# Optimization experiments

Measured on AMD Instinct MI355X. Metric: run time of the kernel, lower is better.

## Reference

```python
import jax, jax.numpy as jnp
import numpy as np
from jax import lax

WINDOW_SIZE = 12
POOL = 4  # AvgPool2d(4): 12x12 -> 3x3

# 4 directional 3x3 kernels, stacked as [O=4, I=1, 3, 3]
_KERNELS = np.stack([
    np.array([[0, 0, 0], [-1, 1, 0], [0, 0, 0]], np.float32),  # left
    np.array([[0, 0, 0], [0, 1, -1], [0, 0, 0]], np.float32),  # right
    np.array([[0, -1, 0], [0, 1, 0], [0, 0, 0]], np.float32),  # up
    np.array([[0, 0, 0], [0, 1, 0], [0, -1, 0]], np.float32),  # down
])[:, None, :, :]


def setup_inputs() -> dict:
    key = jax.random.key(0)
    k1, k2 = jax.random.split(key)
    windows_num = 200000
    n = WINDOW_SIZE * WINDOW_SIZE * windows_num
    samples1 = jax.random.uniform(k1, (n, 3), dtype=jnp.float32)
    samples2 = jax.random.uniform(k2, (n, 3), dtype=jnp.float32)
    return {"samples1": samples1, "samples2": samples2, "windows_num": windows_num}


def _to_pooled(samples, windows_num):
    # [W*W*N, C] -> [W, W, N, C] -> [N, C, W, W]
    x = samples.reshape(WINDOW_SIZE, WINDOW_SIZE, windows_num, -1)
    x = jnp.transpose(x, (2, 3, 0, 1))
    # channel mean, keepdim -> [N, 1, W, W]
    m = jnp.mean(x, axis=1, keepdims=True)
    # AvgPool2d(4): [N,1,12,12] -> [N,1,3,3]
    hp = WINDOW_SIZE // POOL
    p = m.reshape(windows_num, 1, hp, POOL, hp, POOL).mean(axis=(3, 5))
    return p


def _dir_grads(x):
    # x: [N,1,3,3]; 4 directional 3x3 convs, padding=1 -> [N,4,3,3]
    k = jnp.asarray(_KERNELS)
    return lax.conv_general_dilated(
        x, k, window_strides=(1, 1), padding=[(1, 1), (1, 1)],
        dimension_numbers=("NCHW", "OIHW", "NCHW"))


def reference(samples1, samples2, windows_num):
    org_pool = _to_pooled(samples1, windows_num)
    enh_pool = _to_pooled(samples2, windows_num)
    d_org = _dir_grads(org_pool)
    d_enh = _dir_grads(enh_pool)
    # squared diff per direction, summed over the 4 directions -> [N,3,3]
    E = jnp.sum((d_org - d_enh) ** 2, axis=1)
    return jnp.mean(E)
```

## Files before the change

### kernel.cpp

```cpp
#include <hip/hip_runtime.h>

typedef float f32x4 __attribute__((ext_vector_type(4)));

__global__ __launch_bounds__(384) void spa_kernel_p6(
    const float* __restrict__ s1, const float* __restrict__ s2,
    float* __restrict__ out, int N, float scale) {
  const int lane = threadIdx.x & 63;
  const int rg   = threadIdx.x >> 6;
  const int g4   = blockIdx.x * 64 + lane;
  const int nG   = N >> 2;

  float P[4][3];
#pragma unroll
  for (int w = 0; w < 4; ++w)
#pragma unroll
    for (int c = 0; c < 3; ++c) P[w][c] = 0.f;

  if (g4 < nG) {
    const size_t stride = (size_t)N * 3u;
    const size_t rowoff = (size_t)12 * stride;
    const float* p1 = s1 + (size_t)g4 * 12u + (size_t)(rg * 2) * rowoff;
    const float* p2 = s2 + (size_t)g4 * 12u + (size_t)(rg * 2) * rowoff;
#pragma unroll 1
    for (int ii = 0; ii < 2; ++ii) {
#pragma unroll
      for (int j = 0; j < 12; ++j) {
        const f32x4* a = (const f32x4*)(p1 + (size_t)j * stride);
        const f32x4* b = (const f32x4*)(p2 + (size_t)j * stride);
        f32x4 a0 = a[0], a1 = a[1], a2 = a[2];
        f32x4 b0 = b[0], b1 = b[1], b2 = b[2];
        float d0 = (a0.x + a0.y + a0.z) - (b0.x + b0.y + b0.z);
        float d1 = (a0.w + a1.x + a1.y) - (b0.w + b1.x + b1.y);
        float d2 = (a1.z + a1.w + a2.x) - (b1.z + b1.w + b2.x);
        float d3 = (a2.y + a2.z + a2.w) - (b2.y + b2.z + b2.w);
        const int pc = j >> 2;
        P[0][pc] += d0;
        P[1][pc] += d1;
        P[2][pc] += d2;
        P[3][pc] += d3;
      }
      p1 += rowoff;
      p2 += rowoff;
    }
  }

  __shared__ float sP[6][64][13];
#pragma unroll
  for (int w = 0; w < 4; ++w)
#pragma unroll
    for (int c = 0; c < 3; ++c) sP[rg][lane][w * 3 + c] = P[w][c];
  __syncthreads();

  if (rg == 0) {
    float e = 0.f;
#pragma unroll
    for (int w = 0; w < 4; ++w) {
      float Q[9];
#pragma unroll
      for (int pr = 0; pr < 3; ++pr)
#pragma unroll
        for (int c = 0; c < 3; ++c)
          Q[pr * 3 + c] = (sP[2 * pr][lane][w * 3 + c] +
                           sP[2 * pr + 1][lane][w * 3 + c]) * (1.0f / 48.0f);
#pragma unroll
      for (int i = 0; i < 3; ++i)
#pragma unroll
        for (int j = 0; j < 3; ++j) {
          float cc = Q[i * 3 + j];
          float l = (j > 0) ? Q[i * 3 + j - 1] : 0.f;
          float r = (j < 2) ? Q[i * 3 + j + 1] : 0.f;
          float u = (i > 0) ? Q[(i - 1) * 3 + j] : 0.f;
          float d = (i < 2) ? Q[(i + 1) * 3 + j] : 0.f;
          float dl = cc - l, dr = cc - r, du = cc - u, dd = cc - d;
          e += dl * dl + dr * dr + du * du + dd * dd;
        }
    }
#pragma unroll
    for (int off = 32; off > 0; off >>= 1) e += __shfl_down(e, off, 64);
    if (lane == 0) atomicAdd(out, e * scale);
  }
}

__global__ __launch_bounds__(512) void spa_kernel_s(
    const float* __restrict__ s1, const float* __restrict__ s2,
    float* __restrict__ out, int N, float scale) {
  const int win = blockIdx.x * 512 + threadIdx.x;
  float P[9];
#pragma unroll
  for (int k = 0; k < 9; ++k) P[k] = 0.f;

  if (win < N) {
    const size_t stride = (size_t)N * 3u;
    const float* p1 = s1 + (size_t)win * 3u;
    const float* p2 = s2 + (size_t)win * 3u;
#pragma unroll 1
    for (int i = 0; i < 12; ++i) {
      const int pr = (i >> 2) * 3;
#pragma unroll
      for (int j = 0; j < 12; ++j) {
        const float* a = p1 + (size_t)j * stride;
        const float* b = p2 + (size_t)j * stride;
        float d = (a[0] + a[1] + a[2]) - (b[0] + b[1] + b[2]);
        P[pr + (j >> 2)] += d;
      }
      p1 += (size_t)12 * stride;
      p2 += (size_t)12 * stride;
    }
  }

#pragma unroll
  for (int k = 0; k < 9; ++k) P[k] *= (1.0f / 48.0f);

  float e = 0.f;
#pragma unroll
  for (int i = 0; i < 3; ++i)
#pragma unroll
    for (int j = 0; j < 3; ++j) {
      float c = P[i * 3 + j];
      float l = (j > 0) ? P[i * 3 + j - 1] : 0.f;
      float r = (j < 2) ? P[i * 3 + j + 1] : 0.f;
      float u = (i > 0) ? P[(i - 1) * 3 + j] : 0.f;
      float d = (i < 2) ? P[(i + 1) * 3 + j] : 0.f;
      float dl = c - l, dr = c - r, du = c - u, dd = c - d;
      e += dl * dl + dr * dr + du * du + dd * dd;
    }

  const int lane = threadIdx.x & 63;
  const int wid = threadIdx.x >> 6;
#pragma unroll
  for (int off = 32; off > 0; off >>= 1) e += __shfl_down(e, off, 64);

  __shared__ float sPart[8];
  if (lane == 0) sPart[wid] = e;
  __syncthreads();
  if (threadIdx.x == 0) {
    float t = 0.f;
#pragma unroll
    for (int w = 0; w < 8; ++w) t += sPart[w];
    atomicAdd(out, t * scale);
  }
}

extern "C" void kernel_launch(void* const* d_in, const int* in_sizes, int n_in,
                              void* d_out, int out_size, void* d_ws, size_t ws_size,
                              hipStream_t stream) {
  const float* s1 = (const float*)d_in[0];
  const float* s2 = (const float*)d_in[1];
  float* out = (float*)d_out;
  int N = in_sizes[0] / (12 * 12 * 3);
  float scale = 1.0f / (9.0f * (float)N);
  hipMemsetAsync(d_out, 0, sizeof(float), stream);
  if ((N & 3) == 0) {
    int nG = N >> 2;
    int blocks = (nG + 63) / 64;
    spa_kernel_p6<<<blocks, 384, 0, stream>>>(s1, s2, out, N, scale);
  } else {
    int blocks = (N + 511) / 512;
    spa_kernel_s<<<blocks, 512, 0, stream>>>(s1, s2, out, N, scale);
  }
}
```

Before: 668.3 us.

## Remap threads to contiguous float4 columns and transpose partial sums through LDS

Each thread now loads one float4 per row, so adjacent lanes read adjacent 16-byte chunks and every wave access is fully coalesced. The kernel accumulates per-column float4 differences, not per-window channel sums. Per-window channel grouping (three floats per window) is recovered after a shared-memory transpose. Blocks grow to 576 threads in three row groups, and the final reduction goes through an extra barrier plus shared partials. The aim is better memory coalescing for a bandwidth-bound streaming read, at the cost of more LDS traffic and a different occupancy profile.

```diff
diff --git a/kernel.cpp b/kernel.cpp
--- a/kernel.cpp
+++ b/kernel.cpp
@@ -2,83 +2,74 @@
 
 typedef float f32x4 __attribute__((ext_vector_type(4)));
 
-__global__ __launch_bounds__(384) void spa_kernel_p6(
+__global__ __launch_bounds__(576) void spa_kernel_t(
     const float* __restrict__ s1, const float* __restrict__ s2,
     float* __restrict__ out, int N, float scale) {
-  const int lane = threadIdx.x & 63;
-  const int rg   = threadIdx.x >> 6;
-  const int g4   = blockIdx.x * 64 + lane;
-  const int nG   = N >> 2;
+  const int tid  = threadIdx.x;
+  const int col  = tid % 192;
+  const int rg   = tid / 192;
+  const int nF4  = (N >> 2) * 3;
+  const int gcol = blockIdx.x * 192 + col;
 
-  float P[4][3];
+  __shared__ f32x4 L[3][3][192];
+  __shared__ float sPart[4];
+
+  f32x4 A[3];
 #pragma unroll
-  for (int w = 0; w < 4; ++w)
-#pragma unroll
-    for (int c = 0; c < 3; ++c) P[w][c] = 0.f;
+  for (int pc = 0; pc < 3; ++pc) A[pc] = {0.f, 0.f, 0.f, 0.f};
 
-  if (g4 < nG) {
-    const size_t stride = (size_t)N * 3u;
-    const size_t rowoff = (size_t)12 * stride;
-    const float* p1 = s1 + (size_t)g4 * 12u + (size_t)(rg * 2) * rowoff;
-    const float* p2 = s2 + (size_t)g4 * 12u + (size_t)(rg * 2) * rowoff;
+  if (gcol < nF4) {
+    const size_t slab   = (size_t)N * 3u;
+    const size_t rowoff = 12u * slab;
+    const float* p1 = s1 + (size_t)gcol * 4u + (size_t)(rg * 4) * rowoff;
+    const float* p2 = s2 + (size_t)gcol * 4u + (size_t)(rg * 4) * rowoff;
 #pragma unroll 1
-    for (int ii = 0; ii < 2; ++ii) {
-#pragma unroll
+    for (int ii = 0; ii < 4; ++ii) {
+#pragma unroll 6
       for (int j = 0; j < 12; ++j) {
-        const f32x4* a = (const f32x4*)(p1 + (size_t)j * stride);
-        const f32x4* b = (const f32x4*)(p2 + (size_t)j * stride);
-        f32x4 a0 = a[0], a1 = a[1], a2 = a[2];
-        f32x4 b0 = b[0], b1 = b[1], b2 = b[2];
-        float d0 = (a0.x + a0.y + a0.z) - (b0.x + b0.y + b0.z);
-        float d1 = (a0.w + a1.x + a1.y) - (b0.w + b1.x + b1.y);
-        float d2 = (a1.z + a1.w + a2.x) - (b1.z + b1.w + b2.x);
-        float d3 = (a2.y + a2.z + a2.w) - (b2.y + b2.z + b2.w);
-        const int pc = j >> 2;
-        P[0][pc] += d0;
-        P[1][pc] += d1;
-        P[2][pc] += d2;
-        P[3][pc] += d3;
+        f32x4 a = *(const f32x4*)(p1 + (size_t)j * slab);
+        f32x4 b = *(const f32x4*)(p2 + (size_t)j * slab);
+        A[j >> 2] += a - b;
       }
       p1 += rowoff;
       p2 += rowoff;
     }
   }
 
-  __shared__ float sP[6][64][13];
 #pragma unroll
-  for (int w = 0; w < 4; ++w)
-#pragma unroll
-    for (int c = 0; c < 3; ++c) sP[rg][lane][w * 3 + c] = P[w][c];
+  for (int pc = 0; pc < 3; ++pc) L[rg][pc][col] = A[pc];
   __syncthreads();
 
-  if (rg == 0) {
+  if (tid < 256) {
+    const float* Lf = (const float*)L;
     float e = 0.f;
+    float Q[9];
 #pragma unroll
-    for (int w = 0; w < 4; ++w) {
-      float Q[9];
+    for (int pr = 0; pr < 3; ++pr)
 #pragma unroll
-      for (int pr = 0; pr < 3; ++pr)
+      for (int pc = 0; pc < 3; ++pc) {
+        const int base = (pr * 3 + pc) * 768 + 3 * tid;
+        Q[pr * 3 + pc] = (Lf[base] + Lf[base + 1] + Lf[base + 2]) * (1.0f / 48.0f);
+      }
 #pragma unroll
-        for (int c = 0; c < 3; ++c)
-          Q[pr * 3 + c] = (sP[2 * pr][lane][w * 3 + c] +
-                           sP[2 * pr + 1][lane][w * 3 + c]) * (1.0f / 48.0f);
+    for (int i = 0; i < 3; ++i)
 #pragma unroll
-      for (int i = 0; i < 3; ++i)
-#pragma unroll
-        for (int j = 0; j < 3; ++j) {
-          float cc = Q[i * 3 + j];
-          float l = (j > 0) ? Q[i * 3 + j - 1] : 0.f;
-          float r = (j < 2) ? Q[i * 3 + j + 1] : 0.f;
-          float u = (i > 0) ? Q[(i - 1) * 3 + j] : 0.f;
-          float d = (i < 2) ? Q[(i + 1) * 3 + j] : 0.f;
-          float dl = cc - l, dr = cc - r, du = cc - u, dd = cc - d;
-          e += dl * dl + dr * dr + du * du + dd * dd;
-        }
-    }
+      for (int j = 0; j < 3; ++j) {
+        float cc = Q[i * 3 + j];
+        float l = (j > 0) ? Q[i * 3 + j - 1] : 0.f;
+        float r = (j < 2) ? Q[i * 3 + j + 1] : 0.f;
+        float u = (i > 0) ? Q[(i - 1) * 3 + j] : 0.f;
+        float d = (i < 2) ? Q[(i + 1) * 3 + j] : 0.f;
+        float dl = cc - l, dr = cc - r, du = cc - u, dd = cc - d;
+        e += dl * dl + dr * dr + du * du + dd * dd;
+      }
 #pragma unroll
     for (int off = 32; off > 0; off >>= 1) e += __shfl_down(e, off, 64);
-    if (lane == 0) atomicAdd(out, e * scale);
+    if ((tid & 63) == 0) sPart[tid >> 6] = e;
   }
+  __syncthreads();
+  if (tid == 0)
+    atomicAdd(out, (sPart[0] + sPart[1] + sPart[2] + sPart[3]) * scale);
 }
 
 __global__ __launch_bounds__(512) void spa_kernel_s(
@@ -130,13 +121,13 @@
 #pragma unroll
   for (int off = 32; off > 0; off >>= 1) e += __shfl_down(e, off, 64);
 
-  __shared__ float sPart[8];
-  if (lane == 0) sPart[wid] = e;
+  __shared__ float sPartS[8];
+  if (lane == 0) sPartS[wid] = e;
   __syncthreads();
   if (threadIdx.x == 0) {
     float t = 0.f;
 #pragma unroll
-    for (int w = 0; w < 8; ++w) t += sPart[w];
+    for (int w = 0; w < 8; ++w) t += sPartS[w];
     atomicAdd(out, t * scale);
   }
 }
@@ -151,9 +142,9 @@
   float scale = 1.0f / (9.0f * (float)N);
   hipMemsetAsync(d_out, 0, sizeof(float), stream);
   if ((N & 3) == 0) {
-    int nG = N >> 2;
-    int blocks = (nG + 63) / 64;
-    spa_kernel_p6<<<blocks, 384, 0, stream>>>(s1, s2, out, N, scale);
+    int nF4 = (N >> 2) * 3;
+    int blocks = (nF4 + 191) / 192;
+    spa_kernel_t<<<blocks, 576, 0, stream>>>(s1, s2, out, N, scale);
   } else {
     int blocks = (N + 511) / 512;
     spa_kernel_s<<<blocks, 512, 0, stream>>>(s1, s2, out, N, scale);
```

After: 648.8 us. 1.03x faster.
